# Kernel tuning notes

Hardware: AMD Instinct MI355X
Metric: run time of the kernel (lower is better)

Reference implementation:

```python
import jax, jax.numpy as jnp
import numpy as np

B, S, D = 2, 2048, 1024
H, DH = 16, 64  # num_heads, per-head depth (kd//H == vd//H)
NEG = -1e10


def setup_inputs() -> dict:
    key = jax.random.key(0)
    ks = jax.random.split(key, 5)
    scale = 0.02
    return {
        "X": jax.random.normal(ks[0], (B, S, D), dtype=jnp.float32),
        "Wq": jax.random.normal(ks[1], (D, D), dtype=jnp.float32) * scale,
        "Wk": jax.random.normal(ks[2], (D, D), dtype=jnp.float32) * scale,
        "Wv": jax.random.normal(ks[3], (D, D), dtype=jnp.float32) * scale,
        "Wo": jax.random.normal(ks[4], (D, D), dtype=jnp.float32) * scale,
    }


def reference(X, Wq, Wk, Wv, Wo):
    # torch nn.Linear(in,out,bias=False): y = x @ W.T, W is [out,in]
    q = X @ Wq.T  # [B,S,H*DH]
    k = X @ Wk.T
    v = X @ Wv.T
    # split heads -> [B,H,S,DH]
    q = q.reshape(B, S, H, DH).transpose(0, 2, 1, 3) * (DH ** -0.5)
    k = k.reshape(B, S, H, DH).transpose(0, 2, 1, 3)
    v = v.reshape(B, S, H, DH).transpose(0, 2, 1, 3)
    # causal bias: -1e10 on strictly upper triangle (psuedolikelihood=False)
    bias = NEG * jnp.triu(jnp.ones((S, S), dtype=jnp.float32), 1)
    # logits[...,q,k] = q . k
    logits = jnp.einsum("bhkd,bhqd->bhqk", k, q) + bias
    weights = jax.nn.softmax(logits, axis=-1)  # [B,H,S,S]
    out = jnp.einsum("bhqk,bhkd->bhqd", weights, v)
    out = out.transpose(0, 2, 1, 3).reshape(B, S, H * DH)
    return out @ Wo.T  # [B,S,D]
```

## Files before the change

### kernel.cpp

```cpp
#include <hip/hip_runtime.h>
#include <math.h>


typedef _Float16 f16x8 __attribute__((ext_vector_type(8)));
typedef _Float16 f16x4 __attribute__((ext_vector_type(4)));
typedef _Float16 f16x2 __attribute__((ext_vector_type(2)));
typedef __attribute__((ext_vector_type(4))) float f32x4;
typedef __attribute__((ext_vector_type(16))) float f32x16;

#define MFMA16(a, b, c) __builtin_amdgcn_mfma_f32_16x16x32_f16(a, b, c, 0, 0, 0)
#define MFMA32(a, b, c) __builtin_amdgcn_mfma_f32_32x32x16_f16(a, b, c, 0, 0, 0)
#define QSCALE 0.18033688f

__device__ __forceinline__ void async16(const void* g, void* l) {
  __builtin_amdgcn_global_load_lds(
      (const __attribute__((address_space(1))) unsigned int*)g,
      (__attribute__((address_space(3))) unsigned int*)l, 16, 0, 0);
}

__device__ __forceinline__ f16x2 pk2(float x, float y) {
  return __builtin_bit_cast(f16x2, __builtin_amdgcn_cvt_pkrtz(x, y));
}

__device__ __forceinline__ f16x8 cvt8(const float* __restrict__ p) {
  float4 a = *(const float4*)p;
  float4 b = *(const float4*)(p + 4);
  f16x2 p0 = pk2(a.x, a.y), p1 = pk2(a.z, a.w);
  f16x2 p2 = pk2(b.x, b.y), p3 = pk2(b.z, b.w);
  f16x8 h;
  h[0] = p0[0]; h[1] = p0[1]; h[2] = p1[0]; h[3] = p1[1];
  h[4] = p2[0]; h[5] = p2[1]; h[6] = p3[0]; h[7] = p3[1];
  return h;
}

__global__ void convert_all(const float* __restrict__ X, const float* __restrict__ Wq,
                            const float* __restrict__ Wk, const float* __restrict__ Wv,
                            const float* __restrict__ Wo, _Float16* __restrict__ Xh,
                            _Float16* __restrict__ Wqkvh, _Float16* __restrict__ Woh) {
  size_t i = ((size_t)blockIdx.x * 256 + threadIdx.x) * 8;
  const float* src; _Float16* dst; size_t off;
  if (i < 4194304u)      { src = X;  dst = Xh;              off = i; }
  else if (i < 5242880u) { src = Wq; dst = Wqkvh;           off = i - 4194304u; }
  else if (i < 6291456u) { src = Wk; dst = Wqkvh + 1048576; off = i - 5242880u; }
  else if (i < 7340032u) { src = Wv; dst = Wqkvh + 2097152; off = i - 6291456u; }
  else                   { src = Wo; dst = Woh;             off = i - 7340032u; }
  *(f16x8*)(dst + off) = cvt8(src + off);
}

__global__ __launch_bounds__(256) void gemm_qkv_a(
    const _Float16* __restrict__ Xh, const _Float16* __restrict__ Wh,
    _Float16* __restrict__ Qh, _Float16* __restrict__ Kh,
    _Float16* __restrict__ Vth) {
  __shared__ _Float16 As[128 * 32];
  __shared__ _Float16 Bs[128 * 32];
  const int tid = threadIdx.x;
  const int wave = tid >> 6, lane = tid & 63;
  const int quad = lane >> 4, l16 = lane & 15;
  const int wm = (wave >> 1) * 64, wn = (wave & 1) * 64;
  const int bn = blockIdx.x, bm = blockIdx.y;
  const int mat = bn >> 3;

  const int r0 = tid >> 2, cc0 = (tid & 3) * 8;
  const int r1 = (tid + 256) >> 2, cc1 = (tid & 3) * 8;
  const _Float16* gA0 = &Xh[(size_t)(bm * 128 + r0) * 1024 + cc0];
  const _Float16* gA1 = &Xh[(size_t)(bm * 128 + r1) * 1024 + cc1];
  const _Float16* gB0 = &Wh[(size_t)(bn * 128 + r0) * 1024 + cc0];
  const _Float16* gB1 = &Wh[(size_t)(bn * 128 + r1) * 1024 + cc1];

  f32x4 acc[4][4] = {};

  for (int k0 = 0; k0 < 1024; k0 += 32) {
    __syncthreads();
    async16(gA0 + k0, &As[(wave * 64) * 8]);
    async16(gA1 + k0, &As[(256 + wave * 64) * 8]);
    async16(gB0 + k0, &Bs[(wave * 64) * 8]);
    async16(gB1 + k0, &Bs[(256 + wave * 64) * 8]);
    __syncthreads();
    f16x8 af[4], bf[4];
#pragma unroll
    for (int t = 0; t < 4; ++t) {
      af[t] = *(const f16x8*)&As[(wm + t * 16 + l16) * 32 + quad * 8];
      bf[t] = *(const f16x8*)&Bs[(wn + t * 16 + l16) * 32 + quad * 8];
    }
#pragma unroll
    for (int mt = 0; mt < 4; ++mt)
#pragma unroll
      for (int nt = 0; nt < 4; ++nt)
        acc[mt][nt] = MFMA16(af[mt], bf[nt], acc[mt][nt]);
  }

#pragma unroll
  for (int mt = 0; mt < 4; ++mt) {
    int m_base = bm * 128 + wm + mt * 16 + quad * 4;
    int b = m_base >> 11, sb = m_base & 2047;
#pragma unroll
    for (int nt = 0; nt < 4; ++nt) {
      int ob = (bn * 128 + wn + nt * 16) & 1023;
      int h = ob >> 6;
      int dh = (ob & 63) + l16;
      size_t bh = (size_t)(b * 16 + h);
      if (mat == 0) {
#pragma unroll
        for (int r = 0; r < 4; ++r)
          Qh[(bh * 2048 + sb + r) * 64 + dh] = (_Float16)(acc[mt][nt][r] * QSCALE);
      } else if (mat == 1) {
#pragma unroll
        for (int r = 0; r < 4; ++r)
          Kh[(bh * 2048 + sb + r) * 64 + dh] = (_Float16)acc[mt][nt][r];
      } else {
        f16x4 pk;
        pk[0] = (_Float16)acc[mt][nt][0];
        pk[1] = (_Float16)acc[mt][nt][1];
        pk[2] = (_Float16)acc[mt][nt][2];
        pk[3] = (_Float16)acc[mt][nt][3];
        *(f16x4*)&Vth[(bh * 64 + dh) * 2048 + sb] = pk;
      }
    }
  }
}

__global__ __launch_bounds__(256) void gemm_qkv_f(
    const _Float16* __restrict__ Xh, const float* __restrict__ Wq,
    const float* __restrict__ Wk, const float* __restrict__ Wv,
    _Float16* __restrict__ Qh, _Float16* __restrict__ Kh,
    _Float16* __restrict__ Vth) {
  __shared__ _Float16 As[128 * 72];
  __shared__ _Float16 Bs[128 * 72];
  const int tid = threadIdx.x;
  const int wave = tid >> 6, lane = tid & 63;
  const int quad = lane >> 4, l16 = lane & 15;
  const int wm = (wave >> 1) * 64, wn = (wave & 1) * 64;
  const int bn = blockIdx.x, bm = blockIdx.y;
  const int mat = bn >> 3;
  const float* Bsrc = (mat == 0) ? Wq : (mat == 1) ? Wk : Wv;
  const int brow0 = (bn & 7) * 128;

  f32x4 acc[4][4] = {};

  for (int k0 = 0; k0 < 1024; k0 += 64) {
    __syncthreads();
#pragma unroll
    for (int j = 0; j < 4; ++j) {
      int idx = tid + j * 256;
      int row = idx >> 3, c8 = idx & 7;
      *(int4*)&As[row * 72 + c8 * 8] =
          *(const int4*)&Xh[(size_t)(bm * 128 + row) * 1024 + k0 + c8 * 8];
      *(f16x8*)&Bs[row * 72 + c8 * 8] =
          cvt8(&Bsrc[(size_t)(brow0 + row) * 1024 + k0 + c8 * 8]);
    }
    __syncthreads();
#pragma unroll
    for (int kc = 0; kc < 2; ++kc) {
      f16x8 af[4], bf[4];
#pragma unroll
      for (int t = 0; t < 4; ++t) {
        af[t] = *(const f16x8*)&As[(wm + t * 16 + l16) * 72 + kc * 32 + quad * 8];
        bf[t] = *(const f16x8*)&Bs[(wn + t * 16 + l16) * 72 + kc * 32 + quad * 8];
      }
#pragma unroll
      for (int mt = 0; mt < 4; ++mt)
#pragma unroll
        for (int nt = 0; nt < 4; ++nt)
          acc[mt][nt] = MFMA16(af[mt], bf[nt], acc[mt][nt]);
    }
  }

#pragma unroll
  for (int mt = 0; mt < 4; ++mt) {
    int m_base = bm * 128 + wm + mt * 16 + quad * 4;
    int b = m_base >> 11, sb = m_base & 2047;
#pragma unroll
    for (int nt = 0; nt < 4; ++nt) {
      int ob = (bn * 128 + wn + nt * 16) & 1023;
      int h = ob >> 6;
      int dh = (ob & 63) + l16;
      size_t bh = (size_t)(b * 16 + h);
      if (mat == 0) {
#pragma unroll
        for (int r = 0; r < 4; ++r)
          Qh[(bh * 2048 + sb + r) * 64 + dh] = (_Float16)(acc[mt][nt][r] * QSCALE);
      } else if (mat == 1) {
#pragma unroll
        for (int r = 0; r < 4; ++r)
          Kh[(bh * 2048 + sb + r) * 64 + dh] = (_Float16)acc[mt][nt][r];
      } else {
        f16x4 pk;
        pk[0] = (_Float16)acc[mt][nt][0];
        pk[1] = (_Float16)acc[mt][nt][1];
        pk[2] = (_Float16)acc[mt][nt][2];
        pk[3] = (_Float16)acc[mt][nt][3];
        *(f16x4*)&Vth[(bh * 64 + dh) * 2048 + sb] = pk;
      }
    }
  }
}

__global__ __launch_bounds__(512) void attn_kernel(
    const _Float16* __restrict__ Qg, const _Float16* __restrict__ Kg,
    const _Float16* __restrict__ Vtg, _Float16* __restrict__ Og) {
  __shared__ _Float16 smem[2 * (128 * 72 + 64 * 136)];
  const int bh = blockIdx.x;
  const int qt = 15 - (int)blockIdx.y;
  const int q0 = qt * 128;
  const int tid = threadIdx.x;
  const int group = tid >> 8;
  const int tidg = tid & 255;
  const int wv = (tid >> 6) & 3;
  const int lane = tid & 63;
  const int l31 = lane & 31, hl = lane >> 5;
  const int b = bh >> 4, h = bh & 15;
  const int qrow = q0 + wv * 32 + l31;

  _Float16* Kl = smem + group * (128 * 72 + 64 * 136);
  _Float16* Vl = Kl + 128 * 72;

  const _Float16* Qbase = Qg + ((size_t)bh * 2048 + qrow) * 64 + hl * 8;
  f16x8 aq[4];
#pragma unroll
  for (int t = 0; t < 4; ++t) aq[t] = *(const f16x8*)(Qbase + 16 * t);

  f32x16 oacc[2] = {};
  float la = 0.f, lb = 0.f;

  const int krow = tidg >> 3, kc8 = (tidg & 7) * 8;
  const int vrow = tidg >> 4, vc16 = (tidg & 15) * 8;
  const _Float16* gK = Kg + ((size_t)bh * 2048 + krow) * 64 + kc8;
  const _Float16* gV = Vtg + ((size_t)bh * 64 + vrow) * 2048 + vc16;

  int4 ka0, ka1, ka2, ka3, va0, va1, va2, va3;
  {
    const int ktp = (group <= qt) ? group : qt;
    const _Float16* kp = gK + (size_t)ktp * (128 * 64);
    const _Float16* vp = gV + (size_t)ktp * 128;
    ka0 = *(const int4*)(kp + 0 * 32 * 64);
    ka1 = *(const int4*)(kp + 1 * 32 * 64);
    ka2 = *(const int4*)(kp + 2 * 32 * 64);
    ka3 = *(const int4*)(kp + 3 * 32 * 64);
    va0 = *(const int4*)(vp + 0 * 16 * 2048);
    va1 = *(const int4*)(vp + 1 * 16 * 2048);
    va2 = *(const int4*)(vp + 2 * 16 * 2048);
    va3 = *(const int4*)(vp + 3 * 16 * 2048);
  }

  const int nmax = (qt + 2) >> 1;
  for (int it = 0; it < nmax; ++it) {
    const int kt = 2 * it + group;
    const bool valid = (kt <= qt);
    const int k0 = kt << 7;
    __syncthreads();
    *(int4*)&Kl[(krow + 0) * 72 + kc8] = ka0;
    *(int4*)&Kl[(krow + 32) * 72 + kc8] = ka1;
    *(int4*)&Kl[(krow + 64) * 72 + kc8] = ka2;
    *(int4*)&Kl[(krow + 96) * 72 + kc8] = ka3;
    *(int4*)&Vl[(vrow + 0) * 136 + vc16] = va0;
    *(int4*)&Vl[(vrow + 16) * 136 + vc16] = va1;
    *(int4*)&Vl[(vrow + 32) * 136 + vc16] = va2;
    *(int4*)&Vl[(vrow + 48) * 136 + vc16] = va3;
    {
      const int ktn = (kt + 2 <= qt) ? (kt + 2) : qt;
      const _Float16* kp = gK + (size_t)ktn * (128 * 64);
      const _Float16* vp = gV + (size_t)ktn * 128;
      ka0 = *(const int4*)(kp + 0 * 32 * 64);
      ka1 = *(const int4*)(kp + 1 * 32 * 64);
      ka2 = *(const int4*)(kp + 2 * 32 * 64);
      ka3 = *(const int4*)(kp + 3 * 32 * 64);
      va0 = *(const int4*)(vp + 0 * 16 * 2048);
      va1 = *(const int4*)(vp + 1 * 16 * 2048);
      va2 = *(const int4*)(vp + 2 * 16 * 2048);
      va3 = *(const int4*)(vp + 3 * 16 * 2048);
    }
    __syncthreads();
    if (!valid) continue;

    const bool diag = (kt == qt);

#pragma unroll
    for (int s32t = 0; s32t < 4; ++s32t) {
      f32x16 tv = {};
#pragma unroll
      for (int t = 0; t < 4; ++t) {
        f16x8 kb = *(const f16x8*)&Kl[(s32t * 32 + l31) * 72 + t * 16 + hl * 8];
        tv = MFMA32(kb, aq[t], tv);
      }
      int pkx[8];
#pragma unroll
      for (int i = 0; i < 8; ++i) {
        float x0 = tv[2 * i], x1 = tv[2 * i + 1];
        int kg = k0 + s32t * 32 + ((2 * i) & 3) + 8 * (i >> 1) + 4 * hl;
        if (diag) {
          if (kg > qrow) x0 = -1e30f;
          if (kg + 1 > qrow) x1 = -1e30f;
        }
        x0 = __builtin_amdgcn_exp2f(x0);
        x1 = __builtin_amdgcn_exp2f(x1);
        la += x0;
        lb += x1;
        pkx[i] = __builtin_bit_cast(int, pk2(x0, x1));
      }
      int s0 = hl ? pkx[0] : pkx[2];
      int s1 = hl ? pkx[1] : pkx[3];
      int s2 = hl ? pkx[4] : pkx[6];
      int s3 = hl ? pkx[5] : pkx[7];
      int r0 = __shfl_xor(s0, 32);
      int r1 = __shfl_xor(s1, 32);
      int r2 = __shfl_xor(s2, 32);
      int r3 = __shfl_xor(s3, 32);
      int4 f0, f1;
      f0.x = hl ? r0 : pkx[0];
      f0.y = hl ? r1 : pkx[1];
      f0.z = hl ? pkx[2] : r0;
      f0.w = hl ? pkx[3] : r1;
      f1.x = hl ? r2 : pkx[4];
      f1.y = hl ? r3 : pkx[5];
      f1.z = hl ? pkx[6] : r2;
      f1.w = hl ? pkx[7] : r3;
      f16x8 bp0 = __builtin_bit_cast(f16x8, f0);
      f16x8 bp1 = __builtin_bit_cast(f16x8, f1);
#pragma unroll
      for (int d = 0; d < 2; ++d) {
        f16x8 vb0 = *(const f16x8*)&Vl[(d * 32 + l31) * 136 + s32t * 32 + hl * 8];
        f16x8 vb1 =
            *(const f16x8*)&Vl[(d * 32 + l31) * 136 + s32t * 32 + 16 + hl * 8];
        oacc[d] = MFMA32(vb0, bp0, oacc[d]);
        oacc[d] = MFMA32(vb1, bp1, oacc[d]);
      }
    }
  }

  float lsum = la + lb;
  __syncthreads();
  float* mbuf = (float*)(smem + (128 * 72 + 64 * 136));
  float* slot = mbuf + (wv * 64 + lane) * 33;
  if (group == 1) {
#pragma unroll
    for (int d = 0; d < 2; ++d)
#pragma unroll
      for (int j = 0; j < 16; ++j) slot[d * 16 + j] = oacc[d][j];
    slot[32] = lsum;
  }
  __syncthreads();
  if (group == 0) {
#pragma unroll
    for (int d = 0; d < 2; ++d)
#pragma unroll
      for (int j = 0; j < 16; ++j) oacc[d][j] += slot[d * 16 + j];
    lsum += slot[32];
    lsum += __shfl_xor(lsum, 32);
    float inv = 1.0f / lsum;
#pragma unroll
    for (int d = 0; d < 2; ++d)
#pragma unroll
      for (int rq = 0; rq < 4; ++rq) {
        f16x4 o;
#pragma unroll
        for (int j = 0; j < 4; ++j)
          o[j] = (_Float16)(oacc[d][rq * 4 + j] * inv);
        int dh = d * 32 + 8 * rq + 4 * hl;
        *(f16x4*)&Og[(((size_t)b * 2048 + qrow) * 16 + h) * 64 + dh] = o;
      }
  }
}

template <int BH>
__global__ __launch_bounds__(256) void gemm_out(
    const _Float16* __restrict__ A, const float* __restrict__ Wo,
    const _Float16* __restrict__ Woh, float* __restrict__ Co) {
  __shared__ _Float16 As[128 * 72];
  __shared__ _Float16 Bs[64 * 72];
  const int tid = threadIdx.x;
  const int wave = tid >> 6, lane = tid & 63;
  const int quad = lane >> 4, l16 = lane & 15;
  const int wm = (wave >> 1) * 64, wn = (wave & 1) * 32;
  const int bn = blockIdx.x, bm = blockIdx.y;

  f32x4 acc[4][2] = {};

  for (int k0 = 0; k0 < 1024; k0 += 64) {
    __syncthreads();
#pragma unroll
    for (int j = 0; j < 4; ++j) {
      int idx = tid + j * 256;
      int row = idx >> 3, c8 = idx & 7;
      *(int4*)&As[row * 72 + c8 * 8] =
          *(const int4*)&A[(size_t)(bm * 128 + row) * 1024 + k0 + c8 * 8];
    }
#pragma unroll
    for (int j = 0; j < 2; ++j) {
      int idx = tid + j * 256;
      int row = idx >> 3, c8 = idx & 7;
      if (BH)
        *(int4*)&Bs[row * 72 + c8 * 8] =
            *(const int4*)&Woh[(size_t)(bn * 64 + row) * 1024 + k0 + c8 * 8];
      else
        *(f16x8*)&Bs[row * 72 + c8 * 8] =
            cvt8(&Wo[(size_t)(bn * 64 + row) * 1024 + k0 + c8 * 8]);
    }
    __syncthreads();
#pragma unroll
    for (int kc = 0; kc < 2; ++kc) {
      f16x8 af[4], bf[2];
#pragma unroll
      for (int t = 0; t < 4; ++t)
        af[t] = *(const f16x8*)&As[(wm + t * 16 + l16) * 72 + kc * 32 + quad * 8];
#pragma unroll
      for (int t = 0; t < 2; ++t)
        bf[t] = *(const f16x8*)&Bs[(wn + t * 16 + l16) * 72 + kc * 32 + quad * 8];
#pragma unroll
      for (int mt = 0; mt < 4; ++mt)
#pragma unroll
        for (int nt = 0; nt < 2; ++nt)
          acc[mt][nt] = MFMA16(af[mt], bf[nt], acc[mt][nt]);
    }
  }

#pragma unroll
  for (int mt = 0; mt < 4; ++mt) {
    int m_base = bm * 128 + wm + mt * 16 + quad * 4;
#pragma unroll
    for (int nt = 0; nt < 2; ++nt) {
      int n = bn * 64 + wn + nt * 16 + l16;
#pragma unroll
      for (int r = 0; r < 4; ++r)
        Co[(size_t)(m_base + r) * 1024 + n] = acc[mt][nt][r];
    }
  }
}

extern "C" void kernel_launch(void* const* d_in, const int* in_sizes, int n_in,
                              void* d_out, int out_size, void* d_ws, size_t ws_size,
                              hipStream_t stream) {
  const float* X  = (const float*)d_in[0];
  const float* Wq = (const float*)d_in[1];
  const float* Wk = (const float*)d_in[2];
  const float* Wv = (const float*)d_in[3];
  const float* Wo = (const float*)d_in[4];
  float* out = (float*)d_out;

  _Float16* Qh    = (_Float16*)d_out;
  _Float16* Kh    = Qh + 4194304;
  _Float16* Vth   = (_Float16*)d_ws;
  _Float16* Xh    = Vth + 4194304;
  _Float16* Og    = Xh;
  _Float16* Wqkvh = Xh + 4194304;
  _Float16* Woh   = Wqkvh + 3145728;

  const bool big = (ws_size >= 25165824u);

  convert_all<<<big ? 4096 : 2048, 256, 0, stream>>>(X, Wq, Wk, Wv, Wo,
                                                     Xh, Wqkvh, Woh);
  if (big)
    gemm_qkv_a<<<dim3(24, 32), 256, 0, stream>>>(Xh, Wqkvh, Qh, Kh, Vth);
  else
    gemm_qkv_f<<<dim3(24, 32), 256, 0, stream>>>(Xh, Wq, Wk, Wv, Qh, Kh, Vth);
  attn_kernel<<<dim3(32, 16), 512, 0, stream>>>(Qh, Kh, Vth, Og);
  if (big)
    gemm_out<1><<<dim3(16, 32), 256, 0, stream>>>(Og, Wo, Woh, out);
  else
    gemm_out<0><<<dim3(16, 32), 256, 0, stream>>>(Og, Wo, nullptr, out);
}
```

Baseline: 172.6 us.

## Use async global-to-LDS loads in output GEMM and raise MFMA priority in attention

The output projection GEMM on the fp16-weights path is rewritten as a separate kernel. It stages A and W tiles straight into unpadded LDS through global_load_lds async copies, with a K step of 32 instead of 64, which avoids the register round trip. Separately, the attention kernel wraps its two MFMA loops in s_setprio(1)/s_setprio(0) so waves issuing matrix work get scheduling priority over the softmax/exp phase. The unpadded 32-wide LDS layout can cause bank conflicts, and the halved K step doubles the number of barriers per tile.

```diff
diff --git a/kernel.cpp b/kernel.cpp
--- a/kernel.cpp
+++ b/kernel.cpp
@@ -277,11 +277,13 @@
 #pragma unroll
     for (int s32t = 0; s32t < 4; ++s32t) {
       f32x16 tv = {};
+      __builtin_amdgcn_s_setprio(1);
 #pragma unroll
       for (int t = 0; t < 4; ++t) {
         f16x8 kb = *(const f16x8*)&Kl[(s32t * 32 + l31) * 72 + t * 16 + hl * 8];
         tv = MFMA32(kb, aq[t], tv);
       }
+      __builtin_amdgcn_s_setprio(0);
       int pkx[8];
 #pragma unroll
       for (int i = 0; i < 8; ++i) {
@@ -316,6 +318,7 @@
       f1.w = hl ? pkx[7] : r3;
       f16x8 bp0 = __builtin_bit_cast(f16x8, f0);
       f16x8 bp1 = __builtin_bit_cast(f16x8, f1);
+      __builtin_amdgcn_s_setprio(1);
 #pragma unroll
       for (int d = 0; d < 2; ++d) {
         f16x8 vb0 = *(const f16x8*)&Vl[(d * 32 + l31) * 136 + s32t * 32 + hl * 8];
@@ -324,6 +327,7 @@
         oacc[d] = MFMA32(vb0, bp0, oacc[d]);
         oacc[d] = MFMA32(vb1, bp1, oacc[d]);
       }
+      __builtin_amdgcn_s_setprio(0);
     }
   }
 
@@ -361,10 +365,61 @@
   }
 }
 
-template <int BH>
-__global__ __launch_bounds__(256) void gemm_out(
+__global__ __launch_bounds__(256) void gemm_out_a(
+    const _Float16* __restrict__ A, const _Float16* __restrict__ Woh,
+    float* __restrict__ Co) {
+  __shared__ _Float16 As[128 * 32];
+  __shared__ _Float16 Bs[64 * 32];
+  const int tid = threadIdx.x;
+  const int wave = tid >> 6, lane = tid & 63;
+  const int quad = lane >> 4, l16 = lane & 15;
+  const int wm = (wave >> 1) * 64, wn = (wave & 1) * 32;
+  const int bn = blockIdx.x, bm = blockIdx.y;
+
+  const int r0 = tid >> 2, cc0 = (tid & 3) * 8;
+  const int r1 = (tid + 256) >> 2;
+  const _Float16* gA0 = &A[(size_t)(bm * 128 + r0) * 1024 + cc0];
+  const _Float16* gA1 = &A[(size_t)(bm * 128 + r1) * 1024 + cc0];
+  const _Float16* gB0 = &Woh[(size_t)(bn * 64 + r0) * 1024 + cc0];
+
+  f32x4 acc[4][2] = {};
+
+  for (int k0 = 0; k0 < 1024; k0 += 32) {
+    __syncthreads();
+    async16(gA0 + k0, &As[(wave * 64) * 8]);
+    async16(gA1 + k0, &As[(256 + wave * 64) * 8]);
+    if (r0 < 64) async16(gB0 + k0, &Bs[(wave * 64) * 8]);
+    __syncthreads();
+    f16x8 af[4], bf[2];
+#pragma unroll
+    for (int t = 0; t < 4; ++t)
+      af[t] = *(const f16x8*)&As[(wm + t * 16 + l16) * 32 + quad * 8];
+#pragma unroll
+    for (int t = 0; t < 2; ++t)
+      bf[t] = *(const f16x8*)&Bs[(wn + t * 16 + l16) * 32 + quad * 8];
+#pragma unroll
+    for (int mt = 0; mt < 4; ++mt)
+#pragma unroll
+      for (int nt = 0; nt < 2; ++nt)
+        acc[mt][nt] = MFMA16(af[mt], bf[nt], acc[mt][nt]);
+  }
+
+#pragma unroll
+  for (int mt = 0; mt < 4; ++mt) {
+    int m_base = bm * 128 + wm + mt * 16 + quad * 4;
+#pragma unroll
+    for (int nt = 0; nt < 2; ++nt) {
+      int n = bn * 64 + wn + nt * 16 + l16;
+#pragma unroll
+      for (int r = 0; r < 4; ++r)
+        Co[(size_t)(m_base + r) * 1024 + n] = acc[mt][nt][r];
+    }
+  }
+}
+
+__global__ __launch_bounds__(256) void gemm_out_f(
     const _Float16* __restrict__ A, const float* __restrict__ Wo,
-    const _Float16* __restrict__ Woh, float* __restrict__ Co) {
+    float* __restrict__ Co) {
   __shared__ _Float16 As[128 * 72];
   __shared__ _Float16 Bs[64 * 72];
   const int tid = threadIdx.x;
@@ -388,12 +443,8 @@
     for (int j = 0; j < 2; ++j) {
       int idx = tid + j * 256;
       int row = idx >> 3, c8 = idx & 7;
-      if (BH)
-        *(int4*)&Bs[row * 72 + c8 * 8] =
-            *(const int4*)&Woh[(size_t)(bn * 64 + row) * 1024 + k0 + c8 * 8];
-      else
-        *(f16x8*)&Bs[row * 72 + c8 * 8] =
-            cvt8(&Wo[(size_t)(bn * 64 + row) * 1024 + k0 + c8 * 8]);
+      *(f16x8*)&Bs[row * 72 + c8 * 8] =
+          cvt8(&Wo[(size_t)(bn * 64 + row) * 1024 + k0 + c8 * 8]);
     }
     __syncthreads();
 #pragma unroll
@@ -454,7 +505,7 @@
     gemm_qkv_f<<<dim3(24, 32), 256, 0, stream>>>(Xh, Wq, Wk, Wv, Qh, Kh, Vth);
   attn_kernel<<<dim3(32, 16), 512, 0, stream>>>(Qh, Kh, Vth, Og);
   if (big)
-    gemm_out<1><<<dim3(16, 32), 256, 0, stream>>>(Og, Wo, Woh, out);
+    gemm_out_a<<<dim3(16, 32), 256, 0, stream>>>(Og, Woh, out);
   else
-    gemm_out<0><<<dim3(16, 32), 256, 0, stream>>>(Og, Wo, nullptr, out);
-}
+    gemm_out_f<<<dim3(16, 32), 256, 0, stream>>>(Og, Wo, out);
+}
```

After: 175.7 us. About the same (+1.8%).
